# Kernel optimization log

Hardware: AMD Instinct MI355X
Metric: run time of the kernel (lower is better)

Reference implementation:

```python
import jax, jax.numpy as jnp
from jax import lax
import numpy as np

SIGMA = 1.0
TRUNCATE = 3.0

def _gaussian_1d(sigma, truncate):
    tail = int(sigma * truncate)
    x = np.arange(-tail, tail + 1, dtype=np.float32)
    k = np.exp(-0.5 * x * x / (sigma * sigma))
    k = k / k.sum()
    return jnp.asarray(k, dtype=jnp.float32)  # length 2*tail+1 (=7)


def setup_inputs() -> dict:
    key = jax.random.key(0)
    image = jax.random.normal(key, (2, 160, 160, 160, 4), dtype=jnp.float32)
    return {"image": image}


def reference(image):
    # Separable per-channel (depthwise) Gaussian blur along each spatial axis,
    # SAME padding, stride 1 -- identical math to the TF per-channel conv loop.
    k = _gaussian_1d(SIGMA, TRUNCATE)
    K = k.shape[0]
    C = image.shape[-1]
    out = image
    for d in range(3):  # spatial axes D, H, W
        kshape = [1, 1, 1]
        kshape[d] = K
        # depthwise kernel: (kd, kh, kw, in_per_group=1, C)
        rhs = jnp.broadcast_to(k.reshape(kshape + [1, 1]), tuple(kshape) + (1, C))
        out = lax.conv_general_dilated(
            out, rhs,
            window_strides=(1, 1, 1),
            padding='SAME',
            dimension_numbers=('NDHWC', 'DHWIO', 'NDHWC'),
            feature_group_count=C,
        )
    return out
```

## Files before the change

### kernel.cpp

```cpp
#include <hip/hip_runtime.h>


#define THT 16
#define TWT 32
#define CHUNK 16
#define DIM 160
#define SLICE (DIM * DIM)
#define RAWN (22 * 38)
#define NBLK 1000

#define W0 0.004433048f
#define W1 0.054005582f
#define W2 0.242036229f
#define W3 0.399050300f

__device__ __forceinline__ float4 blur7(float4 a0, float4 a1, float4 a2, float4 a3,
                                        float4 a4, float4 a5, float4 a6) {
    float4 r;
    r.x = W0 * (a0.x + a6.x) + W1 * (a1.x + a5.x) + W2 * (a2.x + a4.x) + W3 * a3.x;
    r.y = W0 * (a0.y + a6.y) + W1 * (a1.y + a5.y) + W2 * (a2.y + a4.y) + W3 * a3.y;
    r.z = W0 * (a0.z + a6.z) + W1 * (a1.z + a5.z) + W2 * (a2.z + a4.z) + W3 * a3.z;
    r.w = W0 * (a0.w + a6.w) + W1 * (a1.w + a5.w) + W2 * (a2.w + a4.w) + W3 * a3.w;
    return r;
}

__device__ __forceinline__ void lds_barrier() {
    asm volatile("s_waitcnt lgkmcnt(0)" ::: "memory");
    __builtin_amdgcn_s_barrier();
}

__global__ __launch_bounds__(256, 4)
void gauss3d_fused(const float4* __restrict__ in, float4* __restrict__ out) {
    int work = (blockIdx.x & 7) * (NBLK / 8) + (blockIdx.x >> 3);
    const int tw    = work % (DIM / TWT);   work /= (DIM / TWT);
    const int th    = work % (DIM / THT);   work /= (DIM / THT);
    const int chunk = work % (DIM / CHUNK); work /= (DIM / CHUNK);
    const int n     = work;

    const int h0 = th * THT;
    const int w0 = tw * TWT;
    const int d0 = chunk * CHUNK;

    __shared__ float4 raw[2][22][39];
    __shared__ float4 wb[22][33];

    const int tid = threadIdx.x;
    const size_t nbase = (size_t)n * DIM * SLICE;
    const float4 z = make_float4(0.f, 0.f, 0.f, 0.f);

    int  soff[4], rbidx[4];
    bool sok[4];
    #pragma unroll
    for (int s = 0; s < 4; ++s) {
        const int i = tid + 256 * s;
        const bool has = (i < RAWN);
        const int rr = has ? (i / 38) : 0, cc = has ? (i % 38) : 0;
        const int gh = h0 + rr - 3, gw = w0 + cc - 3;
        const bool ok = has && gh >= 0 && gh < DIM && gw >= 0 && gw < DIM;
        soff[s]  = ok ? (gh * DIM + gw) : 0;
        sok[s]   = ok;
        rbidx[s] = rr * 39 + cc;
    }
    const bool shas3 = (tid + 768 < RAWN);

    const bool isW = (tid < 176);
    const int wr  = tid >> 3;
    const int wc0 = (tid & 7) * 4;

    const int hp = tid >> 5;
    const int lw = tid & 31;

    float4 pf0, pf1, pf2, pf3;
    float4 a0 = z, a1 = z, a2 = z, a3 = z, a4 = z, a5 = z, a6 = z;
    float4 b0 = z, b1 = z, b2 = z, b3 = z, b4 = z, b5 = z, b6 = z;

#define PREFETCH(DSL)                                                        \
    do {                                                                     \
        const int _d = (DSL);                                                \
        const bool _inr = (_d >= 0) && (_d < DIM);                           \
        const float4* _s = in + nbase + (size_t)(_inr ? _d : 0) * SLICE;     \
        pf0 = (_inr && sok[0]) ? _s[soff[0]] : z;                            \
        pf1 = (_inr && sok[1]) ? _s[soff[1]] : z;                            \
        pf2 = (_inr && sok[2]) ? _s[soff[2]] : z;                            \
        pf3 = (_inr && sok[3]) ? _s[soff[3]] : z;                            \
    } while (0)

    PREFETCH(d0 - 3);
    int buf = 0;

    for (int din = d0 - 3; din <= d0 + CHUNK + 2; ++din) {
        {
            float4* rb = &raw[buf][0][0];
            rb[rbidx[0]] = pf0;
            rb[rbidx[1]] = pf1;
            rb[rbidx[2]] = pf2;
            if (shas3) rb[rbidx[3]] = pf3;
        }

        PREFETCH(din + 1);

        lds_barrier();

        if (isW) {
            float4 rv0 = raw[buf][wr][wc0 + 0];
            float4 rv1 = raw[buf][wr][wc0 + 1];
            float4 rv2 = raw[buf][wr][wc0 + 2];
            float4 rv3 = raw[buf][wr][wc0 + 3];
            float4 rv4 = raw[buf][wr][wc0 + 4];
            float4 rv5 = raw[buf][wr][wc0 + 5];
            float4 rv6 = raw[buf][wr][wc0 + 6];
            float4 rv7 = raw[buf][wr][wc0 + 7];
            float4 rv8 = raw[buf][wr][wc0 + 8];
            float4 rv9 = raw[buf][wr][wc0 + 9];
            wb[wr][wc0 + 0] = blur7(rv0, rv1, rv2, rv3, rv4, rv5, rv6);
            wb[wr][wc0 + 1] = blur7(rv1, rv2, rv3, rv4, rv5, rv6, rv7);
            wb[wr][wc0 + 2] = blur7(rv2, rv3, rv4, rv5, rv6, rv7, rv8);
            wb[wr][wc0 + 3] = blur7(rv3, rv4, rv5, rv6, rv7, rv8, rv9);
        }

        lds_barrier();

        {
            float4 c0 = wb[2 * hp + 0][lw];
            float4 c1 = wb[2 * hp + 1][lw];
            float4 c2 = wb[2 * hp + 2][lw];
            float4 c3 = wb[2 * hp + 3][lw];
            float4 c4 = wb[2 * hp + 4][lw];
            float4 c5 = wb[2 * hp + 5][lw];
            float4 c6 = wb[2 * hp + 6][lw];
            float4 c7 = wb[2 * hp + 7][lw];
            float4 va = blur7(c0, c1, c2, c3, c4, c5, c6);
            float4 vb = blur7(c1, c2, c3, c4, c5, c6, c7);
            a0 = a1; a1 = a2; a2 = a3; a3 = a4; a4 = a5; a5 = a6; a6 = va;
            b0 = b1; b1 = b2; b2 = b3; b3 = b4; b4 = b5; b5 = b6; b6 = vb;
        }

        const int dout = din - 3;
        if (dout >= d0) {
            float4 oa = blur7(a0, a1, a2, a3, a4, a5, a6);
            float4 ob = blur7(b0, b1, b2, b3, b4, b5, b6);
            const size_t base = nbase + (size_t)dout * SLICE;
            out[base + (size_t)(h0 + 2 * hp + 0) * DIM + (w0 + lw)] = oa;
            out[base + (size_t)(h0 + 2 * hp + 1) * DIM + (w0 + lw)] = ob;
        }
        buf ^= 1;
    }
#undef PREFETCH
}

extern "C" void kernel_launch(void* const* d_in, const int* in_sizes, int n_in,
                              void* d_out, int out_size, void* d_ws, size_t ws_size,
                              hipStream_t stream) {
    const float4* in = (const float4*)d_in[0];
    float4* out = (float4*)d_out;
    gauss3d_fused<<<NBLK, 256, 0, stream>>>(in, out);
}
```

Measured before the change: 79.86 us.

## Software-pipeline W and H passes with one barrier per slice and fp16 intermediate

Restructures the depth loop so the W-pass for slice k and the H-pass for slice k-1 run in the same iteration, using double-buffered intermediate LDS and one barrier per iteration instead of two. The W-blurred intermediate is stored in LDS as packed half precision to halve its footprint and read bandwidth. This cuts synchronisation stalls and LDS traffic. The price is an extra pipeline iteration, fp16 rounding error in the intermediate, and conversion instructions.

Result: slower. 94.03 us (+17.7%).

```diff
diff --git a/kernel.cpp b/kernel.cpp
--- a/kernel.cpp
+++ b/kernel.cpp
@@ -1,4 +1,5 @@
 #include <hip/hip_runtime.h>
+#include <hip/hip_fp16.h>
 
 
 #define THT 16
@@ -24,6 +25,19 @@
     return r;
 }
 
+__device__ __forceinline__ unsigned h2u(__half2 h) { return *reinterpret_cast<const unsigned*>(&h); }
+
+__device__ __forceinline__ uint2 pack_h4(float4 v) {
+    __half2 a = __floats2half2_rn(v.x, v.y);
+    __half2 b = __floats2half2_rn(v.z, v.w);
+    uint2 r; r.x = h2u(a); r.y = h2u(b); return r;
+}
+__device__ __forceinline__ float4 unpack_h4(uint2 u) {
+    float2 a = __half22float2(*reinterpret_cast<const __half2*>(&u.x));
+    float2 b = __half22float2(*reinterpret_cast<const __half2*>(&u.y));
+    return make_float4(a.x, a.y, b.x, b.y);
+}
+
 __device__ __forceinline__ void lds_barrier() {
     asm volatile("s_waitcnt lgkmcnt(0)" ::: "memory");
     __builtin_amdgcn_s_barrier();
@@ -42,7 +56,7 @@
     const int d0 = chunk * CHUNK;
 
     __shared__ float4 raw[2][22][39];
-    __shared__ float4 wb[22][33];
+    __shared__ uint2  wb[2][22][34];
 
     const int tid = threadIdx.x;
     const size_t nbase = (size_t)n * DIM * SLICE;
@@ -85,67 +99,76 @@
         pf3 = (_inr && sok[3]) ? _s[soff[3]] : z;                            \
     } while (0)
 
+#define COMMIT(BUF)                                                          \
+    do {                                                                     \
+        float4* rb = &raw[BUF][0][0];                                        \
+        rb[rbidx[0]] = pf0;                                                  \
+        rb[rbidx[1]] = pf1;                                                  \
+        rb[rbidx[2]] = pf2;                                                  \
+        if (shas3) rb[rbidx[3]] = pf3;                                       \
+    } while (0)
+
     PREFETCH(d0 - 3);
-    int buf = 0;
+    COMMIT(0);
+    PREFETCH(d0 - 2);
 
-    for (int din = d0 - 3; din <= d0 + CHUNK + 2; ++din) {
-        {
-            float4* rb = &raw[buf][0][0];
-            rb[rbidx[0]] = pf0;
-            rb[rbidx[1]] = pf1;
-            rb[rbidx[2]] = pf2;
-            if (shas3) rb[rbidx[3]] = pf3;
-        }
-
-        PREFETCH(din + 1);
+    for (int k = 0; k <= CHUNK + 6; ++k) {
+        const int s = d0 - 3 + k;
+        const int buf = k & 1;
 
         lds_barrier();
 
-        if (isW) {
-            float4 rv0 = raw[buf][wr][wc0 + 0];
-            float4 rv1 = raw[buf][wr][wc0 + 1];
-            float4 rv2 = raw[buf][wr][wc0 + 2];
-            float4 rv3 = raw[buf][wr][wc0 + 3];
-            float4 rv4 = raw[buf][wr][wc0 + 4];
-            float4 rv5 = raw[buf][wr][wc0 + 5];
-            float4 rv6 = raw[buf][wr][wc0 + 6];
-            float4 rv7 = raw[buf][wr][wc0 + 7];
-            float4 rv8 = raw[buf][wr][wc0 + 8];
-            float4 rv9 = raw[buf][wr][wc0 + 9];
-            wb[wr][wc0 + 0] = blur7(rv0, rv1, rv2, rv3, rv4, rv5, rv6);
-            wb[wr][wc0 + 1] = blur7(rv1, rv2, rv3, rv4, rv5, rv6, rv7);
-            wb[wr][wc0 + 2] = blur7(rv2, rv3, rv4, rv5, rv6, rv7, rv8);
-            wb[wr][wc0 + 3] = blur7(rv3, rv4, rv5, rv6, rv7, rv8, rv9);
+        if (s <= d0 + CHUNK + 2) {
+            if (isW) {
+                float4 rv0 = raw[buf][wr][wc0 + 0];
+                float4 rv1 = raw[buf][wr][wc0 + 1];
+                float4 rv2 = raw[buf][wr][wc0 + 2];
+                float4 rv3 = raw[buf][wr][wc0 + 3];
+                float4 rv4 = raw[buf][wr][wc0 + 4];
+                float4 rv5 = raw[buf][wr][wc0 + 5];
+                float4 rv6 = raw[buf][wr][wc0 + 6];
+                float4 rv7 = raw[buf][wr][wc0 + 7];
+                float4 rv8 = raw[buf][wr][wc0 + 8];
+                float4 rv9 = raw[buf][wr][wc0 + 9];
+                wb[buf][wr][wc0 + 0] = pack_h4(blur7(rv0, rv1, rv2, rv3, rv4, rv5, rv6));
+                wb[buf][wr][wc0 + 1] = pack_h4(blur7(rv1, rv2, rv3, rv4, rv5, rv6, rv7));
+                wb[buf][wr][wc0 + 2] = pack_h4(blur7(rv2, rv3, rv4, rv5, rv6, rv7, rv8));
+                wb[buf][wr][wc0 + 3] = pack_h4(blur7(rv3, rv4, rv5, rv6, rv7, rv8, rv9));
+            }
         }
 
-        lds_barrier();
-
-        {
-            float4 c0 = wb[2 * hp + 0][lw];
-            float4 c1 = wb[2 * hp + 1][lw];
-            float4 c2 = wb[2 * hp + 2][lw];
-            float4 c3 = wb[2 * hp + 3][lw];
-            float4 c4 = wb[2 * hp + 4][lw];
-            float4 c5 = wb[2 * hp + 5][lw];
-            float4 c6 = wb[2 * hp + 6][lw];
-            float4 c7 = wb[2 * hp + 7][lw];
+        if (k >= 1) {
+            const int pb = buf ^ 1;
+            float4 c0 = unpack_h4(wb[pb][2 * hp + 0][lw]);
+            float4 c1 = unpack_h4(wb[pb][2 * hp + 1][lw]);
+            float4 c2 = unpack_h4(wb[pb][2 * hp + 2][lw]);
+            float4 c3 = unpack_h4(wb[pb][2 * hp + 3][lw]);
+            float4 c4 = unpack_h4(wb[pb][2 * hp + 4][lw]);
+            float4 c5 = unpack_h4(wb[pb][2 * hp + 5][lw]);
+            float4 c6 = unpack_h4(wb[pb][2 * hp + 6][lw]);
+            float4 c7 = unpack_h4(wb[pb][2 * hp + 7][lw]);
             float4 va = blur7(c0, c1, c2, c3, c4, c5, c6);
             float4 vb = blur7(c1, c2, c3, c4, c5, c6, c7);
             a0 = a1; a1 = a2; a2 = a3; a3 = a4; a4 = a5; a5 = a6; a6 = va;
             b0 = b1; b1 = b2; b2 = b3; b3 = b4; b4 = b5; b5 = b6; b6 = vb;
+
+            const int dout = s - 4;
+            if (dout >= d0 && dout < d0 + CHUNK) {
+                float4 oa = blur7(a0, a1, a2, a3, a4, a5, a6);
+                float4 ob = blur7(b0, b1, b2, b3, b4, b5, b6);
+                const size_t base = nbase + (size_t)dout * SLICE;
+                out[base + (size_t)(h0 + 2 * hp + 0) * DIM + (w0 + lw)] = oa;
+                out[base + (size_t)(h0 + 2 * hp + 1) * DIM + (w0 + lw)] = ob;
+            }
         }
 
-        const int dout = din - 3;
-        if (dout >= d0) {
-            float4 oa = blur7(a0, a1, a2, a3, a4, a5, a6);
-            float4 ob = blur7(b0, b1, b2, b3, b4, b5, b6);
-            const size_t base = nbase + (size_t)dout * SLICE;
-            out[base + (size_t)(h0 + 2 * hp + 0) * DIM + (w0 + lw)] = oa;
-            out[base + (size_t)(h0 + 2 * hp + 1) * DIM + (w0 + lw)] = ob;
+        if (s + 1 <= d0 + CHUNK + 2) {
+            COMMIT(buf ^ 1);
+            if (s + 2 <= d0 + CHUNK + 2) PREFETCH(s + 2);
         }
-        buf ^= 1;
     }
 #undef PREFETCH
+#undef COMMIT
 }
 
 extern "C" void kernel_launch(void* const* d_in, const int* in_sizes, int n_in,
```

## Stage input slices directly into LDS with async global_load_lds double buffering

Applied to the files above, without the earlier changes.

Replaces the register prefetch plus LDS store of each input depth slice with direct global-to-LDS loads (global_load_lds), double-buffered across iterations with explicit vmcnt waits. The raw tile is flattened to a dense row layout (stride 38), and padding cells are zeroed once up front. The aim is to cut VGPR pressure and the ds_write instructions, and to overlap the next slice load with compute. It adds fragility around vmcnt counting, because the output stores also count against vmcnt, and the dense layout may raise LDS bank conflicts in the W pass.

Result: slower. 100.5 us (+25.8%).

```diff
diff --git a/kernel.cpp b/kernel.cpp
--- a/kernel.cpp
+++ b/kernel.cpp
@@ -4,9 +4,11 @@
 #define THT 16
 #define TWT 32
 #define CHUNK 16
+#define NS (CHUNK + 6)
 #define DIM 160
 #define SLICE (DIM * DIM)
 #define RAWN (22 * 38)
+#define RAWP 864
 #define NBLK 1000
 
 #define W0 0.004433048f
@@ -22,6 +24,13 @@
     r.z = W0 * (a0.z + a6.z) + W1 * (a1.z + a5.z) + W2 * (a2.z + a4.z) + W3 * a3.z;
     r.w = W0 * (a0.w + a6.w) + W1 * (a1.w + a5.w) + W2 * (a2.w + a4.w) + W3 * a3.w;
     return r;
+}
+
+typedef __attribute__((address_space(3))) void lds_void_t;
+typedef const __attribute__((address_space(1))) void gbl_void_t;
+
+__device__ __forceinline__ void gload16(const float4* g, float4* l) {
+    __builtin_amdgcn_global_load_lds((gbl_void_t*)g, (lds_void_t*)l, 16, 0, 0);
 }
 
 __device__ __forceinline__ void lds_barrier() {
@@ -41,15 +50,15 @@
     const int w0 = tw * TWT;
     const int d0 = chunk * CHUNK;
 
-    __shared__ float4 raw[2][22][39];
+    __shared__ float4 raw[2][RAWP];
     __shared__ float4 wb[22][33];
 
     const int tid = threadIdx.x;
     const size_t nbase = (size_t)n * DIM * SLICE;
     const float4 z = make_float4(0.f, 0.f, 0.f, 0.f);
 
-    int  soff[4], rbidx[4];
-    bool sok[4];
+    int  soff[4];
+    bool sok[4], shas[4];
     #pragma unroll
     for (int s = 0; s < 4; ++s) {
         const int i = tid + 256 * s;
@@ -57,61 +66,75 @@
         const int rr = has ? (i / 38) : 0, cc = has ? (i % 38) : 0;
         const int gh = h0 + rr - 3, gw = w0 + cc - 3;
         const bool ok = has && gh >= 0 && gh < DIM && gw >= 0 && gw < DIM;
-        soff[s]  = ok ? (gh * DIM + gw) : 0;
-        sok[s]   = ok;
-        rbidx[s] = rr * 39 + cc;
+        soff[s] = ok ? (gh * DIM + gw) : 0;
+        sok[s]  = ok;
+        shas[s] = has;
     }
-    const bool shas3 = (tid + 768 < RAWN);
+
+    #pragma unroll
+    for (int s = 0; s < 4; ++s) {
+        if (shas[s] && !sok[s]) {
+            raw[0][tid + 256 * s] = z;
+            raw[1][tid + 256 * s] = z;
+        }
+    }
 
     const bool isW = (tid < 176);
     const int wr  = tid >> 3;
     const int wc0 = (tid & 7) * 4;
+    const int wbase = wr * 38 + wc0;
 
     const int hp = tid >> 5;
     const int lw = tid & 31;
 
-    float4 pf0, pf1, pf2, pf3;
     float4 a0 = z, a1 = z, a2 = z, a3 = z, a4 = z, a5 = z, a6 = z;
     float4 b0 = z, b1 = z, b2 = z, b3 = z, b4 = z, b5 = z, b6 = z;
 
-#define PREFETCH(DSL)                                                        \
+    const int wavebase = tid & ~63;
+
+#define STAGE(BUF, DSL)                                                      \
     do {                                                                     \
         const int _d = (DSL);                                                \
-        const bool _inr = (_d >= 0) && (_d < DIM);                           \
-        const float4* _s = in + nbase + (size_t)(_inr ? _d : 0) * SLICE;     \
-        pf0 = (_inr && sok[0]) ? _s[soff[0]] : z;                            \
-        pf1 = (_inr && sok[1]) ? _s[soff[1]] : z;                            \
-        pf2 = (_inr && sok[2]) ? _s[soff[2]] : z;                            \
-        pf3 = (_inr && sok[3]) ? _s[soff[3]] : z;                            \
+        if (_d >= 0 && _d < DIM) {                                           \
+            const float4* _g = in + nbase + (size_t)_d * SLICE;              \
+            float4* _lw = &raw[BUF][wavebase];                               \
+            if (sok[0]) gload16(_g + soff[0], _lw + 0);                      \
+            if (sok[1]) gload16(_g + soff[1], _lw + 256);                    \
+            if (sok[2]) gload16(_g + soff[2], _lw + 512);                    \
+            if (sok[3]) gload16(_g + soff[3], _lw + 768);                    \
+        } else {                                                             \
+            if (sok[0]) raw[BUF][tid + 0]   = z;                             \
+            if (sok[1]) raw[BUF][tid + 256] = z;                             \
+            if (sok[2]) raw[BUF][tid + 512] = z;                             \
+            if (sok[3]) raw[BUF][tid + 768] = z;                             \
+        }                                                                    \
     } while (0)
 
-    PREFETCH(d0 - 3);
-    int buf = 0;
+    STAGE(0, d0 - 3);
 
-    for (int din = d0 - 3; din <= d0 + CHUNK + 2; ++din) {
-        {
-            float4* rb = &raw[buf][0][0];
-            rb[rbidx[0]] = pf0;
-            rb[rbidx[1]] = pf1;
-            rb[rbidx[2]] = pf2;
-            if (shas3) rb[rbidx[3]] = pf3;
-        }
+    for (int k = 0; k < NS; ++k) {
+        const int din = d0 - 3 + k;
+        const int buf = k & 1;
 
-        PREFETCH(din + 1);
+        if (k <= 6) { asm volatile("s_waitcnt vmcnt(0)" ::: "memory"); }
+        else        { asm volatile("s_waitcnt vmcnt(2)" ::: "memory"); }
 
         lds_barrier();
 
+        if (k + 1 < NS) STAGE(buf ^ 1, din + 1);
+
         if (isW) {
-            float4 rv0 = raw[buf][wr][wc0 + 0];
-            float4 rv1 = raw[buf][wr][wc0 + 1];
-            float4 rv2 = raw[buf][wr][wc0 + 2];
-            float4 rv3 = raw[buf][wr][wc0 + 3];
-            float4 rv4 = raw[buf][wr][wc0 + 4];
-            float4 rv5 = raw[buf][wr][wc0 + 5];
-            float4 rv6 = raw[buf][wr][wc0 + 6];
-            float4 rv7 = raw[buf][wr][wc0 + 7];
-            float4 rv8 = raw[buf][wr][wc0 + 8];
-            float4 rv9 = raw[buf][wr][wc0 + 9];
+            const float4* rb = &raw[buf][0];
+            float4 rv0 = rb[wbase + 0];
+            float4 rv1 = rb[wbase + 1];
+            float4 rv2 = rb[wbase + 2];
+            float4 rv3 = rb[wbase + 3];
+            float4 rv4 = rb[wbase + 4];
+            float4 rv5 = rb[wbase + 5];
+            float4 rv6 = rb[wbase + 6];
+            float4 rv7 = rb[wbase + 7];
+            float4 rv8 = rb[wbase + 8];
+            float4 rv9 = rb[wbase + 9];
             wb[wr][wc0 + 0] = blur7(rv0, rv1, rv2, rv3, rv4, rv5, rv6);
             wb[wr][wc0 + 1] = blur7(rv1, rv2, rv3, rv4, rv5, rv6, rv7);
             wb[wr][wc0 + 2] = blur7(rv2, rv3, rv4, rv5, rv6, rv7, rv8);
@@ -135,17 +158,16 @@
             b0 = b1; b1 = b2; b2 = b3; b3 = b4; b4 = b5; b5 = b6; b6 = vb;
         }
 
-        const int dout = din - 3;
-        if (dout >= d0) {
+        if (k >= 6) {
+            const int dout = din - 3;
             float4 oa = blur7(a0, a1, a2, a3, a4, a5, a6);
             float4 ob = blur7(b0, b1, b2, b3, b4, b5, b6);
             const size_t base = nbase + (size_t)dout * SLICE;
             out[base + (size_t)(h0 + 2 * hp + 0) * DIM + (w0 + lw)] = oa;
             out[base + (size_t)(h0 + 2 * hp + 1) * DIM + (w0 + lw)] = ob;
         }
-        buf ^= 1;
     }
-#undef PREFETCH
+#undef STAGE
 }
 
 extern "C" void kernel_launch(void* const* d_in, const int* in_sizes, int n_in,
```
